# Optimization experiments

Measured on AMD Instinct MI355X. Metric: run time of the kernel, lower is better.

The kernel has to match this reference:

```python
import jax, jax.numpy as jnp
import numpy as np

HEADS = 16
DIM_HEAD = 64
SCALE = DIM_HEAD ** -0.5


def setup_inputs() -> dict:
    key = jax.random.key(0)
    ks = jax.random.split(key, 5)
    b, n, dim = 2, 2048, 1024
    inner = HEADS * DIM_HEAD  # 1024
    std = dim ** -0.5
    return {
        "x": jax.random.normal(ks[0], (b, n, dim), jnp.float32),
        "ln_gamma": jnp.ones((dim,), jnp.float32),
        "ln_beta": jnp.zeros((dim,), jnp.float32),
        "W_qk": jax.random.normal(ks[1], (dim, 2 * inner), jnp.float32) * std,
        "W_v": jax.random.normal(ks[2], (dim, inner), jnp.float32) * std,
        "W_out": jax.random.normal(ks[3], (inner, dim), jnp.float32) * std,
        "b_out": jnp.zeros((dim,), jnp.float32),
    }


def _layernorm(x, gamma, beta, eps=1e-5):
    mu = jnp.mean(x, axis=-1, keepdims=True)
    var = jnp.var(x, axis=-1, keepdims=True)
    return (x - mu) * jax.lax.rsqrt(var + eps) * gamma + beta


def reference(x, ln_gamma, ln_beta, W_qk, W_v, W_out, b_out):
    b, n, dim = x.shape
    h, d = HEADS, DIM_HEAD
    xn = _layernorm(x, ln_gamma, ln_beta)
    qk = xn @ W_qk                      # [b, n, 2*h*d]
    q, k = jnp.split(qk, 2, axis=-1)    # each [b, n, h*d]
    v = xn @ W_v                        # [b, n, h*d]
    # b n (h d) -> b h n d
    q = q.reshape(b, n, h, d).transpose(0, 2, 1, 3)
    k = k.reshape(b, n, h, d).transpose(0, 2, 1, 3)
    v = v.reshape(b, n, h, d).transpose(0, 2, 1, 3)
    dots = jnp.einsum('bhid,bhjd->bhij', q, k) * SCALE
    attn = jax.nn.softmax(dots, axis=-1)
    out = jnp.einsum('bhij,bhjd->bhid', attn, v)
    out = out.transpose(0, 2, 1, 3).reshape(b, n, h * d)
    return out @ W_out + b_out
```

## Files before the change

### kernel.cpp

```cpp
#include <hip/hip_runtime.h>

#define HEADS 16
#define DHEAD 64
#define BATCH 2
#define SEQ   2048
#define DIM   1024
#define ROWS  (BATCH*SEQ)
#define SCALE_LOG2E 0.180336880f

typedef short v8s __attribute__((ext_vector_type(8)));
typedef float v4f __attribute__((ext_vector_type(4)));

__device__ __forceinline__ float fast_exp2(float x) {
    return __builtin_amdgcn_exp2f(x);
}

__device__ __forceinline__ unsigned short f2bf(float f) {
    unsigned u = __float_as_uint(f);
    u += 0x7FFFu + ((u >> 16) & 1u);
    return (unsigned short)(u >> 16);
}

__device__ __forceinline__ unsigned pk_bf2(float hi, float lo) {
    return __builtin_amdgcn_perm(__float_as_uint(hi), __float_as_uint(lo), 0x07060302u);
}

#define GLDS16(g, l) __builtin_amdgcn_global_load_lds( \
    (__attribute__((address_space(1))) void*)(g), \
    (__attribute__((address_space(3))) void*)(l), 16, 0, 0)

__global__ __launch_bounds__(256) void ln_kernel(const float* __restrict__ x,
                                                 const float* __restrict__ gamma,
                                                 const float* __restrict__ beta,
                                                 unsigned short* __restrict__ xn) {
    int row = blockIdx.x;
    const float* xr = x + (size_t)row * DIM;
    int t = threadIdx.x;
    float4 v = *(const float4*)(xr + t * 4);
    float s  = v.x + v.y + v.z + v.w;
    float sq = v.x * v.x + v.y * v.y + v.z * v.z + v.w * v.w;
#pragma unroll
    for (int off = 32; off > 0; off >>= 1) {
        s  += __shfl_down(s,  off, 64);
        sq += __shfl_down(sq, off, 64);
    }
    __shared__ float ss[4], ssq[4];
    int wave = t >> 6, lane = t & 63;
    if (lane == 0) { ss[wave] = s; ssq[wave] = sq; }
    __syncthreads();
    float tot  = ss[0] + ss[1] + ss[2] + ss[3];
    float totq = ssq[0] + ssq[1] + ssq[2] + ssq[3];
    float mean = tot * (1.f / DIM);
    float var  = totq * (1.f / DIM) - mean * mean;
    float rstd = rsqrtf(var + 1e-5f);
    float4 g = *(const float4*)(gamma + t * 4);
    float4 bb = *(const float4*)(beta + t * 4);
    ushort4 o;
    o.x = f2bf((v.x - mean) * rstd * g.x + bb.x);
    o.y = f2bf((v.y - mean) * rstd * g.y + bb.y);
    o.z = f2bf((v.z - mean) * rstd * g.z + bb.z);
    o.w = f2bf((v.w - mean) * rstd * g.w + bb.w);
    *(ushort4*)(xn + (size_t)row * DIM + t * 4) = o;
}

__global__ __launch_bounds__(256) void tr_all_kernel(const float* __restrict__ Wqk,
                                                     const float* __restrict__ Wv,
                                                     const float* __restrict__ Wout,
                                                     unsigned short* __restrict__ Tqk,
                                                     unsigned short* __restrict__ Tv,
                                                     unsigned short* __restrict__ To) {
    int z = blockIdx.z;
    const float* W = (z == 0) ? Wqk : (z == 1) ? Wv : Wout;
    unsigned short* Wt = (z == 0) ? Tqk : (z == 1) ? Tv : To;
    int Nw = (z == 0) ? 2048 : 1024;
    int n0 = blockIdx.x * 64, k0 = blockIdx.y * 64;
    if (n0 >= Nw) return;
    __shared__ float tile[64][65];
    int tid = threadIdx.x;
#pragma unroll
    for (int l = 0; l < 4; ++l) {
        int kk = (tid >> 4) + l * 16;
        int nn = (tid & 15) * 4;
        float4 v = *(const float4*)(W + (size_t)(k0 + kk) * Nw + n0 + nn);
        tile[kk][nn + 0] = v.x; tile[kk][nn + 1] = v.y;
        tile[kk][nn + 2] = v.z; tile[kk][nn + 3] = v.w;
    }
    __syncthreads();
#pragma unroll
    for (int l = 0; l < 4; ++l) {
        int cid = tid + l * 256;
        int nn = cid >> 4, kc = (cid & 15) * 4;
        ushort4 o;
        o.x = f2bf(tile[kc + 0][nn]);
        o.y = f2bf(tile[kc + 1][nn]);
        o.z = f2bf(tile[kc + 2][nn]);
        o.w = f2bf(tile[kc + 3][nn]);
        *(ushort4*)(Wt + (size_t)(n0 + nn) * DIM + k0 + kc) = o;
    }
}

template<int BN, bool SWAP>
__device__ __forceinline__ void mm_core2(const unsigned short* __restrict__ A,
                                         const unsigned short* __restrict__ Bt,
                                         int K, int aTile, int bTile,
                                         unsigned short (*As)[32],
                                         unsigned short (*Bs)[32],
                                         v4f (*acc)[4]) {
    constexpr int MI = (BN == 128) ? 4 : 2;
    int t = threadIdx.x;
    int w = t >> 6, L = t & 63, l15 = L & 15, quad = L >> 4;
    int aOff = (BN == 128) ? (w >> 1) * 64 : w * 32;
    int bOff = (BN == 128) ? (w & 1) * 64 : 0;
    int srow = L >> 2, schunk = (L & 3) * 8;
    for (int k0 = 0; k0 < K; k0 += 32) {
        __syncthreads();
#pragma unroll
        for (int j = 0; j < 2; ++j) {
            int g = w * 2 + j;
            GLDS16(A + (size_t)(aTile + g * 16 + srow) * K + k0 + schunk,
                   &As[g * 16][0]);
        }
#pragma unroll
        for (int j = 0; j < BN / 64; ++j) {
            int g = (BN == 128) ? (w * 2 + j) : w;
            GLDS16(Bt + (size_t)(bTile + g * 16 + srow) * K + k0 + schunk,
                   &Bs[g * 16][0]);
        }
        __syncthreads();
        v8s a[MI], b[4];
#pragma unroll
        for (int i = 0; i < MI; ++i) a[i] = *(const v8s*)&As[aOff + i * 16 + l15][quad * 8];
#pragma unroll
        for (int j = 0; j < 4; ++j) b[j] = *(const v8s*)&Bs[bOff + j * 16 + l15][quad * 8];
#pragma unroll
        for (int i = 0; i < MI; ++i)
#pragma unroll
            for (int j = 0; j < 4; ++j)
                acc[i][j] = SWAP
                    ? __builtin_amdgcn_mfma_f32_16x16x32_bf16(b[j], a[i], acc[i][j], 0, 0, 0)
                    : __builtin_amdgcn_mfma_f32_16x16x32_bf16(a[i], b[j], acc[i][j], 0, 0, 0);
    }
}

__global__ __launch_bounds__(256) void gemm_qkv_kernel(const unsigned short* __restrict__ A,
                                                       const unsigned short* __restrict__ Bt,
                                                       unsigned short* __restrict__ q_h,
                                                       unsigned short* __restrict__ k_h,
                                                       unsigned short* __restrict__ v_t) {
    __shared__ __align__(16) unsigned short As[128][32];
    __shared__ __align__(16) unsigned short Bs[128][32];
    int t = threadIdx.x, w = t >> 6, L = t & 63, l15 = L & 15, quad = L >> 4;
    int aTile = blockIdx.y * 128, bTile = blockIdx.x * 128;
    int aOff = (w >> 1) * 64, bOff = (w & 1) * 64;
    v4f acc[4][4] = {};
    if (bTile < 2048) {
        mm_core2<128, true>(A, Bt, DIM, aTile, bTile, As, Bs, acc);
        float sc = (bTile < 1024) ? SCALE_LOG2E : 1.0f;
#pragma unroll
        for (int j = 0; j < 4; ++j) {
            int col = bTile + bOff + j * 16 + quad * 4;
            unsigned short* dst = (col < 1024) ? q_h : k_h;
            int c = col & 1023;
            int h = c >> 6, d = c & 63;
#pragma unroll
            for (int i = 0; i < 4; ++i) {
                int m = aTile + aOff + i * 16 + l15;
                int b = m >> 11, seq = m & 2047;
                ushort4 o;
                o.x = f2bf(acc[i][j][0] * sc); o.y = f2bf(acc[i][j][1] * sc);
                o.z = f2bf(acc[i][j][2] * sc); o.w = f2bf(acc[i][j][3] * sc);
                *(ushort4*)(dst + (((size_t)(b * 16 + h)) * SEQ + seq) * 64 + d) = o;
            }
        }
    } else {
        mm_core2<128, false>(A, Bt, DIM, aTile, bTile, As, Bs, acc);
#pragma unroll
        for (int j = 0; j < 4; ++j) {
            int c = bTile + bOff + j * 16 + l15 - 2048;
            int h = c >> 6, d = c & 63;
#pragma unroll
            for (int i = 0; i < 4; ++i) {
                int m0 = aTile + aOff + i * 16 + quad * 4;
                int b = m0 >> 11, seq0 = m0 & 2047;
                ushort4 o;
                o.x = f2bf(acc[i][j][0]); o.y = f2bf(acc[i][j][1]);
                o.z = f2bf(acc[i][j][2]); o.w = f2bf(acc[i][j][3]);
                *(ushort4*)(v_t + (((size_t)(b * 16 + h)) * 64 + d) * SEQ + seq0) = o;
            }
        }
    }
}

__global__ __launch_bounds__(256) void gemm_out_kernel(const unsigned short* __restrict__ A,
                                                       const unsigned short* __restrict__ Bt,
                                                       const float* __restrict__ bias,
                                                       float* __restrict__ C) {
    __shared__ __align__(16) unsigned short As[128][32];
    __shared__ __align__(16) unsigned short Bs[64][32];
    int t = threadIdx.x, w = t >> 6, L = t & 63, l15 = L & 15, quad = L >> 4;
    int aTile = blockIdx.y * 128, bTile = blockIdx.x * 64;
    v4f acc[2][4] = {};
    mm_core2<64, true>(A, Bt, DIM, aTile, bTile, As, Bs, acc);
#pragma unroll
    for (int j = 0; j < 4; ++j) {
        int n = bTile + j * 16 + quad * 4;
        float4 bv = *(const float4*)(bias + n);
#pragma unroll
        for (int i = 0; i < 2; ++i) {
            int m = aTile + w * 32 + i * 16 + l15;
            float4 o = make_float4(acc[i][j][0] + bv.x, acc[i][j][1] + bv.y,
                                   acc[i][j][2] + bv.z, acc[i][j][3] + bv.w);
            *(float4*)(C + (size_t)m * DIM + n) = o;
        }
    }
}

__global__ __launch_bounds__(512, 4) void attn_kernel(const unsigned short* __restrict__ q_h,
                                                      const unsigned short* __restrict__ k_h,
                                                      const unsigned short* __restrict__ v_t,
                                                      unsigned short* __restrict__ ao) {
    __shared__ __align__(16) unsigned short KF[2][8 * 64 * 8];
    __shared__ __align__(16) unsigned short VF[2][8 * 64 * 8];
    __shared__ __align__(16) unsigned short Pld[8][16 * 72];
    int bid = blockIdx.x;
    int wg = (bid & 7) * 64 + (bid >> 3);
    int qt = wg & 15, h = (wg >> 4) & 15, b = wg >> 8;
    int bh = b * HEADS + h;
    int w = threadIdx.x >> 6;
    int L = threadIdx.x & 63, l15 = L & 15, quad = L >> 4;

    const unsigned short* qp = q_h + ((size_t)bh * SEQ + qt * 128 + w * 16 + l15) * 64 + quad * 8;
    v8s qf0 = *(const v8s*)(qp);
    v8s qf1 = *(const v8s*)(qp + 32);

    const unsigned short* ksrc = k_h + ((size_t)bh * SEQ + (w >> 1) * 16 + l15) * 64 + (w & 1) * 32 + quad * 8;
    const unsigned short* vsrc = v_t + ((size_t)bh * 64 + (w >> 1) * 16 + l15) * SEQ + (w & 1) * 32 + quad * 8;

    GLDS16(ksrc, &KF[0][w * 512]);
    GLDS16(vsrc, &VF[0][w * 512]);

    v4f o[4] = {};
    v4f lacc = {};
    const short ob = (short)0x3F80;
    const v8s ones = {ob, ob, ob, ob, ob, ob, ob, ob};

    int cur = 0;
    for (int j0 = 0; j0 < SEQ; j0 += 64) {
        __syncthreads();
        if (j0 + 64 < SEQ) {
            GLDS16(ksrc + (size_t)(j0 + 64) * 64, &KF[cur ^ 1][w * 512]);
            GLDS16(vsrc + (j0 + 64),              &VF[cur ^ 1][w * 512]);
        }
        v8s kf[4][2], vf[4][2];
#pragma unroll
        for (int jt = 0; jt < 4; ++jt) {
            kf[jt][0] = *(const v8s*)&KF[cur][((jt * 2 + 0) * 64 + L) * 8];
            kf[jt][1] = *(const v8s*)&KF[cur][((jt * 2 + 1) * 64 + L) * 8];
            vf[jt][0] = *(const v8s*)&VF[cur][((jt * 2 + 0) * 64 + L) * 8];
            vf[jt][1] = *(const v8s*)&VF[cur][((jt * 2 + 1) * 64 + L) * 8];
        }
        v4f s[4] = {};
        __builtin_amdgcn_s_setprio(1);
#pragma unroll
        for (int jt = 0; jt < 4; ++jt) {
            s[jt] = __builtin_amdgcn_mfma_f32_16x16x32_bf16(kf[jt][0], qf0, s[jt], 0, 0, 0);
            s[jt] = __builtin_amdgcn_mfma_f32_16x16x32_bf16(kf[jt][1], qf1, s[jt], 0, 0, 0);
        }
        __builtin_amdgcn_s_setprio(0);
#pragma unroll
        for (int jt = 0; jt < 4; ++jt) {
            float p0 = fast_exp2(s[jt][0]);
            float p1 = fast_exp2(s[jt][1]);
            float p2 = fast_exp2(s[jt][2]);
            float p3 = fast_exp2(s[jt][3]);
            uint2 pk;
            pk.x = pk_bf2(p1, p0);
            pk.y = pk_bf2(p3, p2);
            *(uint2*)&Pld[w][l15 * 72 + jt * 16 + quad * 4] = pk;
        }
        v8s pb0 = *(const v8s*)&Pld[w][l15 * 72 + quad * 8];
        v8s pb1 = *(const v8s*)&Pld[w][l15 * 72 + 32 + quad * 8];
        __builtin_amdgcn_s_setprio(1);
#pragma unroll
        for (int dt = 0; dt < 4; ++dt) {
            o[dt] = __builtin_amdgcn_mfma_f32_16x16x32_bf16(vf[dt][0], pb0, o[dt], 0, 0, 0);
            o[dt] = __builtin_amdgcn_mfma_f32_16x16x32_bf16(vf[dt][1], pb1, o[dt], 0, 0, 0);
        }
        lacc = __builtin_amdgcn_mfma_f32_16x16x32_bf16(ones, pb0, lacc, 0, 0, 0);
        lacc = __builtin_amdgcn_mfma_f32_16x16x32_bf16(ones, pb1, lacc, 0, 0, 0);
        __builtin_amdgcn_s_setprio(0);
        cur ^= 1;
    }
    float inv = 1.f / lacc[0];
    int rowg = b * SEQ + qt * 128 + w * 16 + l15;
#pragma unroll
    for (int dt = 0; dt < 4; ++dt) {
        ushort4 ov;
        ov.x = f2bf(o[dt][0] * inv);
        ov.y = f2bf(o[dt][1] * inv);
        ov.z = f2bf(o[dt][2] * inv);
        ov.w = f2bf(o[dt][3] * inv);
        *(ushort4*)(ao + (size_t)rowg * DIM + h * 64 + dt * 16 + quad * 4) = ov;
    }
}

extern "C" void kernel_launch(void* const* d_in, const int* in_sizes, int n_in,
                              void* d_out, int out_size, void* d_ws, size_t ws_size,
                              hipStream_t stream) {
    const float* x     = (const float*)d_in[0];
    const float* gamma = (const float*)d_in[1];
    const float* beta  = (const float*)d_in[2];
    const float* Wqk   = (const float*)d_in[3];
    const float* Wv    = (const float*)d_in[4];
    const float* Wout  = (const float*)d_in[5];
    const float* bout  = (const float*)d_in[6];
    float* out = (float*)d_out;

    unsigned short* ws = (unsigned short*)d_ws;
    unsigned short* xn    = ws;
    unsigned short* Wt_qk = xn + (size_t)ROWS * DIM;
    unsigned short* Wt_v  = Wt_qk + (size_t)2048 * DIM;
    unsigned short* Wt_o  = Wt_v + (size_t)DIM * DIM;
    unsigned short* q_h   = Wt_o + (size_t)DIM * DIM;
    unsigned short* k_h   = q_h + (size_t)ROWS * DIM;
    unsigned short* v_t   = k_h + (size_t)ROWS * DIM;
    unsigned short* ao    = v_t + (size_t)ROWS * DIM;

    ln_kernel<<<ROWS, 256, 0, stream>>>(x, gamma, beta, xn);
    tr_all_kernel<<<dim3(32, 16, 3), 256, 0, stream>>>(Wqk, Wv, Wout, Wt_qk, Wt_v, Wt_o);
    gemm_qkv_kernel<<<dim3(3072 / 128, ROWS / 128), 256, 0, stream>>>(xn, Wt_qk, q_h, k_h, v_t);
    attn_kernel<<<dim3(SEQ / 128 * HEADS * BATCH), 512, 0, stream>>>(q_h, k_h, v_t, ao);
    gemm_out_kernel<<<dim3(DIM / 64, ROWS / 128), 256, 0, stream>>>(ao, Wt_o, bout, out);
}
```

Before: 196.2 us.

## Triple-buffer K/V tiles and software-pipeline QK^T one tile ahead

Moves from double to triple buffering of the K and V LDS tiles, prefetching two tiles ahead. The QK^T MFMAs for the next tile now run while the exp2 of the current tile is computed, so matrix and transcendental work can overlap. This adds LDS use (about 16KB more per block), which may lower occupancy against the launch bound of 4 blocks, and it adds register pressure from keeping the sn accumulators live.

Measured after the change: 195.5 us. About the same (-0.4%).

```diff
diff --git a/kernel.cpp b/kernel.cpp
--- a/kernel.cpp
+++ b/kernel.cpp
@@ -219,8 +219,8 @@
                                                       const unsigned short* __restrict__ k_h,
                                                       const unsigned short* __restrict__ v_t,
                                                       unsigned short* __restrict__ ao) {
-    __shared__ __align__(16) unsigned short KF[2][8 * 64 * 8];
-    __shared__ __align__(16) unsigned short VF[2][8 * 64 * 8];
+    __shared__ __align__(16) unsigned short KF[3][8 * 64 * 8];
+    __shared__ __align__(16) unsigned short VF[3][8 * 64 * 8];
     __shared__ __align__(16) unsigned short Pld[8][16 * 72];
     int bid = blockIdx.x;
     int wg = (bid & 7) * 64 + (bid >> 3);
@@ -236,37 +236,39 @@
     const unsigned short* ksrc = k_h + ((size_t)bh * SEQ + (w >> 1) * 16 + l15) * 64 + (w & 1) * 32 + quad * 8;
     const unsigned short* vsrc = v_t + ((size_t)bh * 64 + (w >> 1) * 16 + l15) * SEQ + (w & 1) * 32 + quad * 8;
 
-    GLDS16(ksrc, &KF[0][w * 512]);
-    GLDS16(vsrc, &VF[0][w * 512]);
+    GLDS16(ksrc,           &KF[0][w * 512]);
+    GLDS16(vsrc,           &VF[0][w * 512]);
+    GLDS16(ksrc + 64 * 64, &KF[1][w * 512]);
+    GLDS16(vsrc + 64,      &VF[1][w * 512]);
 
     v4f o[4] = {};
     v4f lacc = {};
     const short ob = (short)0x3F80;
     const v8s ones = {ob, ob, ob, ob, ob, ob, ob, ob};
 
-    int cur = 0;
-    for (int j0 = 0; j0 < SEQ; j0 += 64) {
-        __syncthreads();
-        if (j0 + 64 < SEQ) {
-            GLDS16(ksrc + (size_t)(j0 + 64) * 64, &KF[cur ^ 1][w * 512]);
-            GLDS16(vsrc + (j0 + 64),              &VF[cur ^ 1][w * 512]);
-        }
-        v8s kf[4][2], vf[4][2];
+    __syncthreads();
+
+    v4f s[4] = {};
+    {
+        v8s kf[4][2];
 #pragma unroll
         for (int jt = 0; jt < 4; ++jt) {
-            kf[jt][0] = *(const v8s*)&KF[cur][((jt * 2 + 0) * 64 + L) * 8];
-            kf[jt][1] = *(const v8s*)&KF[cur][((jt * 2 + 1) * 64 + L) * 8];
-            vf[jt][0] = *(const v8s*)&VF[cur][((jt * 2 + 0) * 64 + L) * 8];
-            vf[jt][1] = *(const v8s*)&VF[cur][((jt * 2 + 1) * 64 + L) * 8];
-        }
-        v4f s[4] = {};
-        __builtin_amdgcn_s_setprio(1);
+            kf[jt][0] = *(const v8s*)&KF[0][((jt * 2 + 0) * 64 + L) * 8];
+            kf[jt][1] = *(const v8s*)&KF[0][((jt * 2 + 1) * 64 + L) * 8];
+        }
 #pragma unroll
         for (int jt = 0; jt < 4; ++jt) {
             s[jt] = __builtin_amdgcn_mfma_f32_16x16x32_bf16(kf[jt][0], qf0, s[jt], 0, 0, 0);
             s[jt] = __builtin_amdgcn_mfma_f32_16x16x32_bf16(kf[jt][1], qf1, s[jt], 0, 0, 0);
         }
-        __builtin_amdgcn_s_setprio(0);
+    }
+
+    int cb = 0, nb = 1, fb = 2;
+    for (int t = 0; t < SEQ / 64; ++t) {
+        if (t + 2 < SEQ / 64) {
+            GLDS16(ksrc + (size_t)(t + 2) * 64 * 64, &KF[fb][w * 512]);
+            GLDS16(vsrc + (t + 2) * 64,              &VF[fb][w * 512]);
+        }
 #pragma unroll
         for (int jt = 0; jt < 4; ++jt) {
             float p0 = fast_exp2(s[jt][0]);
@@ -278,8 +280,30 @@
             pk.y = pk_bf2(p3, p2);
             *(uint2*)&Pld[w][l15 * 72 + jt * 16 + quad * 4] = pk;
         }
+        v4f sn[4] = {};
+        if (t + 1 < SEQ / 64) {
+            v8s kn[4][2];
+#pragma unroll
+            for (int jt = 0; jt < 4; ++jt) {
+                kn[jt][0] = *(const v8s*)&KF[nb][((jt * 2 + 0) * 64 + L) * 8];
+                kn[jt][1] = *(const v8s*)&KF[nb][((jt * 2 + 1) * 64 + L) * 8];
+            }
+            __builtin_amdgcn_s_setprio(1);
+#pragma unroll
+            for (int jt = 0; jt < 4; ++jt) {
+                sn[jt] = __builtin_amdgcn_mfma_f32_16x16x32_bf16(kn[jt][0], qf0, sn[jt], 0, 0, 0);
+                sn[jt] = __builtin_amdgcn_mfma_f32_16x16x32_bf16(kn[jt][1], qf1, sn[jt], 0, 0, 0);
+            }
+            __builtin_amdgcn_s_setprio(0);
+        }
         v8s pb0 = *(const v8s*)&Pld[w][l15 * 72 + quad * 8];
         v8s pb1 = *(const v8s*)&Pld[w][l15 * 72 + 32 + quad * 8];
+        v8s vf[4][2];
+#pragma unroll
+        for (int dt = 0; dt < 4; ++dt) {
+            vf[dt][0] = *(const v8s*)&VF[cb][((dt * 2 + 0) * 64 + L) * 8];
+            vf[dt][1] = *(const v8s*)&VF[cb][((dt * 2 + 1) * 64 + L) * 8];
+        }
         __builtin_amdgcn_s_setprio(1);
 #pragma unroll
         for (int dt = 0; dt < 4; ++dt) {
@@ -289,7 +313,10 @@
         lacc = __builtin_amdgcn_mfma_f32_16x16x32_bf16(ones, pb0, lacc, 0, 0, 0);
         lacc = __builtin_amdgcn_mfma_f32_16x16x32_bf16(ones, pb1, lacc, 0, 0, 0);
         __builtin_amdgcn_s_setprio(0);
-        cur ^= 1;
+#pragma unroll
+        for (int jt = 0; jt < 4; ++jt) s[jt] = sn[jt];
+        int tmp = cb; cb = nb; nb = fb; fb = tmp;
+        __syncthreads();
     }
     float inv = 1.f / lacc[0];
     int rowg = b * SEQ + qt * 128 + w * 16 + l15;
```
